# Performance work log

Measured on AMD Instinct MI355X. Metric: run time of the kernel, lower is better.

The kernel has to match this reference:

```python
import jax, jax.numpy as jnp
import numpy as np

RES = 64

TRI_TABLE = jnp.array([
    [-1,-1,-1,-1,-1,-1],[1,0,2,-1,-1,-1],[4,0,3,-1,-1,-1],[1,4,2,1,3,4],
    [3,1,5,-1,-1,-1],[2,3,0,2,5,3],[1,4,0,1,5,4],[4,2,5,-1,-1,-1],
    [4,5,2,-1,-1,-1],[4,1,0,4,5,1],[3,2,0,3,5,2],[1,3,5,-1,-1,-1],
    [4,1,2,4,3,1],[3,0,4,-1,-1,-1],[2,0,1,-1,-1,-1],[-1,-1,-1,-1,-1,-1]], dtype=jnp.int32)
NUM_TRI = jnp.array([0,1,1,2,1,2,2,1,1,2,2,1,2,1,1,0], dtype=jnp.int32)
BASE_EDGES = jnp.array([0,1,0,2,0,3,1,2,1,3,2,3], dtype=jnp.int32)


def _make_tet_grid(res):
    # Kuhn 6-tet decomposition of each cube of a (res+1)^3 grid.
    n = res + 1
    ii, jj, kk = np.meshgrid(np.arange(n), np.arange(n), np.arange(n), indexing='ij')
    verts = (np.stack([ii, jj, kk], -1).reshape(-1, 3).astype(np.float32)) / res
    def vid(i, j, k):
        return (i * n + j) * n + k
    i, j, k = np.meshgrid(np.arange(res), np.arange(res), np.arange(res), indexing='ij')
    i, j, k = i.ravel(), j.ravel(), k.ravel()
    c = [vid(i + (b & 1), j + ((b >> 1) & 1), k + ((b >> 2) & 1)) for b in range(8)]
    kuhn = [(0,1,3,7),(0,3,2,7),(0,2,6,7),(0,6,4,7),(0,4,5,7),(0,5,1,7)]
    tets = np.stack([np.stack([c[a], c[b], c[d], c[e]], -1) for (a, b, d, e) in kuhn], 1)
    return verts, tets.reshape(-1, 4).astype(np.int64)


def setup_inputs() -> dict:
    key = jax.random.key(0)
    verts, tets = _make_tet_grid(RES)
    level = jax.random.normal(key, (verts.shape[0], 1), dtype=jnp.float32)
    return {"level": level, "pos": jnp.asarray(verts), "tet": jnp.asarray(tets), "threshold": 0}


def reference(level, pos, tet, threshold):
    sdf = level - threshold                    # [N,1]
    occ = sdf[:, 0] > 0                        # [N]
    occ_fx4 = occ[tet]                         # [F,4]
    occ_sum = occ_fx4.sum(-1)
    valid = (occ_sum > 0) & (occ_sum < 4)
    vt = tet[valid]                            # [Fv,4]
    occ_valid = occ_fx4[valid]                 # [Fv,4]

    edges = jnp.sort(vt[:, BASE_EDGES].reshape(-1, 2), axis=1)   # [Fv*6,2]
    unique_edges, idx_map = jnp.unique(edges, axis=0, return_inverse=True)
    idx_map = idx_map.reshape(-1)
    mask_edges = occ[unique_edges].sum(-1) == 1                  # crossing edges
    mapping = jnp.where(mask_edges, jnp.cumsum(mask_edges) - 1, -1)
    idx_map = mapping[idx_map].reshape(-1, 6)                    # [Fv,6]
    interp_v = unique_edges[mask_edges]                          # [M,2]

    p = pos[interp_v]                                            # [M,2,3]
    s = sdf[interp_v][..., 0] * jnp.array([1.0, -1.0], dtype=sdf.dtype)  # [M,2]
    w = s[:, ::-1] / s.sum(1, keepdims=True)                     # flip / denom
    verts_out = (p * w[..., None]).sum(1)                        # [M,3]

    v_id = 2 ** jnp.arange(4, dtype=jnp.int32)
    tetindex = (occ_valid.astype(jnp.int32) * v_id).sum(-1)      # [Fv]
    num_tri = NUM_TRI[tetindex]
    m1, m2 = num_tri == 1, num_tri == 2
    f1 = jnp.take_along_axis(idx_map[m1], TRI_TABLE[tetindex[m1]][:, :3], axis=1).reshape(-1, 3)
    f2 = jnp.take_along_axis(idx_map[m2], TRI_TABLE[tetindex[m2]][:, :6], axis=1).reshape(-1, 3)
    faces = jnp.concatenate([f1, f2], axis=0)
    return verts_out, faces
```

## Files before the change

### kernel.cpp

```cpp
#include <hip/hip_runtime.h>


#define RESX 64
#define NV   65
#define NV2  4225
#define NVERT 274625
#define NCUBE 262144
#define BLOCK 256
#define NGRP 1073
#define CGRP 1024
#define NBLK1 269
#define CBLK 1024
#define FOLD (NGRP - CBLK)
#define WINW 20
#define STAGE 9216
#define M21 0x1fffffu

__constant__ int c_tri[16][6] = {
    {-1,-1,-1,-1,-1,-1},{1,0,2,-1,-1,-1},{4,0,3,-1,-1,-1},{1,4,2,1,3,4},
    {3,1,5,-1,-1,-1},{2,3,0,2,5,3},{1,4,0,1,5,4},{4,2,5,-1,-1,-1},
    {4,5,2,-1,-1,-1},{4,1,0,4,5,1},{3,2,0,3,5,2},{1,3,5,-1,-1,-1},
    {4,1,2,4,3,1},{3,0,4,-1,-1,-1},{2,0,1,-1,-1,-1},{-1,-1,-1,-1,-1,-1}};
__constant__ int c_ntri[16] = {0,1,1,2,1,2,2,1,1,2,2,1,2,1,1,0};
__constant__ int c_kuhn[6][4] = {{0,1,3,7},{0,3,2,7},{0,2,6,7},{0,6,4,7},{0,4,5,7},{0,5,1,7}};
__constant__ int c_off8[8] = {0,4225,65,4290,1,4226,66,4291};
__constant__ int c_loc[6][6] = {
    {0,0,0,1,1,3},{0,0,0,2,3,2},{0,0,0,2,2,6},
    {0,0,0,4,6,4},{0,0,0,4,4,5},{0,0,0,1,5,1}};
__constant__ int c_dir[6][6] = {
    {3,5,6,1,2,0},{5,1,6,3,0,4},{1,2,6,0,4,3},
    {2,0,6,1,3,5},{0,4,6,3,5,1},{4,3,6,0,1,2}};

typedef unsigned long long u64;
#define NTRI_PACK 0x16696994u

__device__ __forceinline__ u64 block_reduce_u64(u64 v, u64* lds) {
    int tid = threadIdx.x, lane = tid & 63, w = tid >> 6;
#pragma unroll
    for (int off = 32; off > 0; off >>= 1)
        v += __shfl_xor(v, off, 64);
    if (lane == 0) lds[w] = v;
    __syncthreads();
    if (tid == 0) lds[4] = lds[0] + lds[1] + lds[2] + lds[3];
    __syncthreads();
    return lds[4];
}

__device__ __forceinline__ unsigned block_scan_excl(unsigned val, unsigned* lds,
                                                    unsigned& block_total) {
    int tid = threadIdx.x, lane = tid & 63, w = tid >> 6;
    unsigned x = val;
#pragma unroll
    for (int off = 1; off < 64; off <<= 1) {
        unsigned y = (unsigned)__shfl_up((int)x, off, 64);
        if (lane >= off) x += y;
    }
    if (lane == 63) lds[w] = x;
    __syncthreads();
    if (tid == 0) {
        unsigned s = 0;
#pragma unroll
        for (int i = 0; i < 4; i++) { unsigned t = lds[i]; lds[i + 4] = s; s += t; }
        lds[8] = s;
    }
    __syncthreads();
    block_total = lds[8];
    return x - val + lds[4 + w];
}

__global__ void __launch_bounds__(256)
pass1(const float* __restrict__ level, const float* __restrict__ thrp,
      unsigned char* __restrict__ flagsArr, unsigned short* __restrict__ locEx,
      u64* __restrict__ bsAll) {
    int tid = threadIdx.x, lane = tid & 63, w = tid >> 6;
    int group = blockIdx.x * 4 + w;
    if (group >= NGRP) return;
    float thr = thrp[0];

    int v = group * 256 + lane * 4;
    unsigned fl[4] = {0, 0, 0, 0};
    if (v <= NVERT - 4295) {
        float r0[5], rY[5], rX[5], rXY[5];
#pragma unroll
        for (int e = 0; e < 5; e++) {
            r0[e]  = level[v + e]        - thr;
            rY[e]  = level[v + 65 + e]   - thr;
            rX[e]  = level[v + 4225 + e] - thr;
            rXY[e] = level[v + 4290 + e] - thr;
        }
        int i0 = v / NV2; int r = v - i0 * NV2; int j0 = r / NV; int k0 = r - j0 * NV;
#pragma unroll
        for (int d = 0; d < 4; d++) {
            int kk = k0 + d, jj = j0;
            if (kk > 64) { kk -= 65; jj += 1; }
            if (jj > 64) { jj -= 65; }
            bool oky = jj < RESX, okz = kk < RESX;
            bool s0 = r0[d] > 0.f;
            unsigned f = s0 ? 0x80u : 0u;
            if (okz &&        ((r0[d+1]  > 0.f) != s0)) f |= 1u;
            if (oky &&        ((rY[d]    > 0.f) != s0)) f |= 2u;
            if (oky && okz && ((rY[d+1]  > 0.f) != s0)) f |= 4u;
            if (              ((rX[d]    > 0.f) != s0)) f |= 8u;
            if (okz &&        ((rX[d+1]  > 0.f) != s0)) f |= 16u;
            if (oky &&        ((rXY[d]   > 0.f) != s0)) f |= 32u;
            if (oky && okz && ((rXY[d+1] > 0.f) != s0)) f |= 64u;
            fl[d] = f;
        }
    } else {
        const int b2d[8] = {0, 3, 1, 5, 0, 4, 2, 6};
#pragma unroll
        for (int d = 0; d < 4; d++) {
            int g = v + d;
            if (g >= NVERT) continue;
            int i = g / NV2; int r = g - i * NV2; int j = r / NV; int k = r - j * NV;
            bool okx = i < RESX, oky = j < RESX, okz = k < RESX;
            float s = level[g] - thr;
            bool s0 = s > 0.f;
            unsigned f = s0 ? 0x80u : 0u;
#pragma unroll
            for (int b = 1; b < 8; b++) {
                bool ok = (!(b & 1) || okx) && (!(b & 2) || oky) && (!(b & 4) || okz);
                if (ok) {
                    float vb = level[g + c_off8[b]] - thr;
                    if ((vb > 0.f) != s0) f |= (1u << b2d[b]);
                }
            }
            fl[d] = f;
        }
    }
    unsigned cnt[4];
#pragma unroll
    for (int d = 0; d < 4; d++) cnt[d] = __popc(fl[d] & 0x7fu);
    unsigned cth = cnt[0] + cnt[1] + cnt[2] + cnt[3];
    unsigned x = cth;
#pragma unroll
    for (int off = 1; off < 64; off <<= 1) {
        unsigned y = (unsigned)__shfl_up((int)x, off, 64);
        if (lane >= off) x += y;
    }
    unsigned wex = x - cth;
    unsigned totE = (unsigned)__shfl((int)x, 63, 64);
    if (v + 3 < NVERT) {
        *(uchar4*)(flagsArr + v) = make_uchar4((unsigned char)fl[0], (unsigned char)fl[1],
                                               (unsigned char)fl[2], (unsigned char)fl[3]);
        ushort4 e4;
        e4.x = (unsigned short)wex;
        e4.y = (unsigned short)(wex + cnt[0]);
        e4.z = (unsigned short)(wex + cnt[0] + cnt[1]);
        e4.w = (unsigned short)(wex + cnt[0] + cnt[1] + cnt[2]);
        *(ushort4*)(locEx + v) = e4;
    } else {
        unsigned e = wex;
        for (int d = 0; d < 4; d++) {
            int g = v + d;
            if (g < NVERT) {
                flagsArr[g] = (unsigned char)fl[d];
                locEx[g] = (unsigned short)e;
                e += cnt[d];
            }
        }
    }

    unsigned c1 = 0, c2 = 0;
    if (group < CGRP) {
        int c0 = group * 256 + lane * 4;
        int ci = c0 >> 12, cj = (c0 >> 6) & 63, ck = c0 & 63;
        int base = (ci * NV + cj) * NV + ck;
        float q0[5], qY[5], qX[5], qXY[5];
#pragma unroll
        for (int e = 0; e < 5; e++) {
            q0[e]  = level[base + e]        - thr;
            qY[e]  = level[base + 65 + e]   - thr;
            qX[e]  = level[base + 4225 + e] - thr;
            qXY[e] = level[base + 4290 + e] - thr;
        }
#pragma unroll
        for (int d = 0; d < 4; d++) {
            unsigned occ8 = (q0[d]   > 0.f ?   1u : 0u) | (qX[d]   > 0.f ?   2u : 0u)
                          | (qY[d]   > 0.f ?   4u : 0u) | (qXY[d]  > 0.f ?   8u : 0u)
                          | (q0[d+1] > 0.f ?  16u : 0u) | (qX[d+1] > 0.f ?  32u : 0u)
                          | (qY[d+1] > 0.f ?  64u : 0u) | (qXY[d+1]> 0.f ? 128u : 0u);
#pragma unroll
            for (int t = 0; t < 6; t++) {
                int cfg = ((occ8 >> c_kuhn[t][0]) & 1) | (((occ8 >> c_kuhn[t][1]) & 1) << 1)
                        | (((occ8 >> c_kuhn[t][2]) & 1) << 2) | (((occ8 >> c_kuhn[t][3]) & 1) << 3);
                unsigned nt = (NTRI_PACK >> (cfg << 1)) & 3u;
                c1 += (nt == 1);
                c2 += (nt == 2);
            }
        }
        unsigned pk = c1 | (c2 << 16);
#pragma unroll
        for (int off = 32; off; off >>= 1) pk += (unsigned)__shfl_xor((int)pk, off, 64);
        c1 = pk & 0xffffu; c2 = pk >> 16;
    }
    if (lane == 0)
        bsAll[group] = (u64)totE | ((u64)c1 << 16) | ((u64)c2 << 32);
}

__device__ __forceinline__ void emit_verts_group(
        int g, unsigned pE, const float* __restrict__ level, float thr,
        const unsigned char* __restrict__ flagsArr,
        const unsigned short* __restrict__ locEx,
        const u64* __restrict__ bsAll, float* stage, float* __restrict__ out,
        const float* cv ) {
    int tid = threadIdx.x;
    int gid = g * BLOCK + tid;
    float lv[8];
    if (cv == nullptr) {
        int gsafe = (gid < NVERT) ? gid : 0;
#pragma unroll
        for (int b = 0; b < 8; b++) {
            int a = gsafe + c_off8[b];
            lv[b] = level[a < NVERT ? a : 0] - thr;
        }
    } else {
#pragma unroll
        for (int b = 0; b < 8; b++) lv[b] = cv[b];
    }
    if (gid < NVERT) {
        unsigned fl = flagsArr[gid];
        if (fl & 0x7fu) {
            int i = gid / NV2; int r = gid - i * NV2; int j = r / NV; int k = r - j * NV;
            float v0 = lv[0];
            unsigned slot = locEx[gid];
            const float inv = 1.f / 64.f;
            const int d2b[7] = {4, 2, 6, 1, 5, 3, 7};
            float fi = (float)i, fj = (float)j, fk = (float)k;
#pragma unroll
            for (int d = 0; d < 7; d++) {
                if (fl & (1u << d)) {
                    const int b = d2b[d];
                    float s1 = lv[b];
                    float w1 = v0 * __builtin_amdgcn_rcpf(v0 - s1);
                    float* o = &stage[3u * slot];
                    o[0] = (fi + (float)(b & 1) * w1) * inv;
                    o[1] = (fj + (float)((b >> 1) & 1) * w1) * inv;
                    o[2] = (fk + (float)((b >> 2) & 1) * w1) * inv;
                    slot++;
                }
            }
        }
    }
    __syncthreads();
    unsigned totE = (unsigned)bsAll[g] & 0xffffu;
    float* dst = out + 3u * pE;
    unsigned n = totE * 3u;
    for (unsigned idx = tid; idx < n; idx += BLOCK)
        __builtin_nontemporal_store(stage[idx], &dst[idx]);
}

__global__ void __launch_bounds__(256)
pass2(const float* __restrict__ level, const float* __restrict__ thrp,
      const unsigned char* __restrict__ flagsArr,
      const unsigned short* __restrict__ locEx,
      const u64* __restrict__ bsAll, float* __restrict__ out) {
    __shared__ unsigned lds[9];
    __shared__ u64 lds64[5];
    __shared__ unsigned win[WINW];
    __shared__ unsigned pEw[WINW];
    __shared__ float stage[STAGE];
    int tid = threadIdx.x;
    int bid = blockIdx.x;
    int gid = bid * BLOCK + tid;
    float thr = thrp[0];
    bool hasB = (bid < FOLD);
    int gB = bid + CBLK;

    int g0 = bid << 8;
    int wci = g0 >> 12, wcj = (g0 >> 6) & 63;
    int wb = ((wci * NV + wcj) * NV) >> 8;

    unsigned lE = 0, lEp = 0, lEpB = 0, lWb = 0, l1 = 0, l1p = 0, l2p = 0;
    for (int t = tid; t < NGRP; t += BLOCK) {
        u64 a = bsAll[t];
        unsigned e  = (unsigned)a & 0xffffu;
        unsigned x1 = (unsigned)(a >> 16) & 0xffffu;
        unsigned x2 = (unsigned)(a >> 32) & 0xffffu;
        lE += e; l1 += x1;
        if (t < bid) { lEp += e; l1p += x1; l2p += x2; }
        if (t < gB)  { lEpB += e; }
        if (t < wb)  { lWb += e; }
    }
    if (tid < WINW) {
        int t = wb + tid;
        win[tid] = (t < NGRP) ? ((unsigned)bsAll[t] & 0xffffu) : 0u;
    }
    float cv[8];
    {
        int gsafe = (gid < NVERT) ? gid : 0;
#pragma unroll
        for (int b = 0; b < 8; b++) {
            int a = gsafe + c_off8[b];
            cv[b] = level[a < NVERT ? a : 0] - thr;
        }
    }
    u64 r0 = block_reduce_u64((u64)lE | ((u64)lEp << 21) | ((u64)lWb << 42), lds64);
    u64 r1 = block_reduce_u64((u64)l1 | ((u64)l1p << 21) | ((u64)l2p << 42), lds64);
    u64 r2 = block_reduce_u64((u64)lEpB, lds64);
    unsigned M    = (unsigned)r0 & M21;
    unsigned pE   = (unsigned)(r0 >> 21) & M21;
    unsigned wAcc = (unsigned)(r0 >> 42);
    unsigned C1   = (unsigned)r1 & M21;
    unsigned p1b  = (unsigned)(r1 >> 21) & M21;
    unsigned p2b  = (unsigned)(r1 >> 42);
    unsigned pEB  = (unsigned)r2;
    if (tid < WINW) {
        unsigned s = wAcc;
        for (int d = 0; d < tid; d++) s += win[d];
        pEw[tid] = s;
    }

    emit_verts_group(bid, pE, level, thr, flagsArr, locEx, bsAll, stage, out, cv);
    if (hasB) {
        __syncthreads();
        emit_verts_group(gB, pEB, level, thr, flagsArr, locEx, bsAll, stage, out,
                         nullptr);
    }
    __syncthreads();

    int ci = gid >> 12, cj = (gid >> 6) & 63, ck = gid & 63;
    int base = (ci * NV + cj) * NV + ck;
    u64 f8 = 0ull;
#pragma unroll
    for (int b = 0; b < 8; b++)
        f8 |= (u64)flagsArr[base + c_off8[b]] << (8 * b);
    unsigned occ8 = 0;
#pragma unroll
    for (int b = 0; b < 8; b++) occ8 |= (unsigned)((f8 >> (8 * b + 7)) & 1ull) << b;
    int cfgs[6], nts[6];
    unsigned c1 = 0, c2 = 0;
#pragma unroll
    for (int t = 0; t < 6; t++) {
        int cfg = ((occ8 >> c_kuhn[t][0]) & 1) | (((occ8 >> c_kuhn[t][1]) & 1) << 1)
                | (((occ8 >> c_kuhn[t][2]) & 1) << 2) | (((occ8 >> c_kuhn[t][3]) & 1) << 3);
        cfgs[t] = cfg;
        int nt = c_ntri[cfg];
        nts[t] = nt;
        c1 += (nt == 1); c2 += (nt == 2);
    }
    unsigned tot2;
    unsigned ex2 = block_scan_excl(c1 | (c2 << 16), lds, tot2);
    unsigned f1 = tot2 & 0xffffu;
    unsigned f2 = tot2 >> 16;
    unsigned l1c = ex2 & 0xffffu;
    unsigned l2c = ex2 >> 16;
    unsigned n1 = f1 * 3u;
#pragma unroll
    for (int t = 0; t < 6; t++) {
        int nt = nts[t];
        if (nt == 0) continue;
        int cfg = cfgs[t];
        unsigned basef = (nt == 1) ? (3u * l1c) : (n1 + 6u * l2c);
        int cntm = 3 * nt;
        for (int m = 0; m < cntm; m++) {
            int e = c_tri[cfg][m];
            int lc = c_loc[t][e];
            int dir = c_dir[t][e];
            int lo = base + c_off8[lc];
            unsigned flb = (unsigned)((f8 >> (8 * lc)) & 0xffull);
            unsigned rnk = pEw[(lo >> 8) - wb] + locEx[lo]
                         + __popc(flb & ((1u << dir) - 1u));
            stage[basef + (unsigned)m] = (float)rnk;
        }
        l1c += (nt == 1);
        l2c += (nt == 2);
    }
    __syncthreads();
    float* of = out + 3ull * M;
    float* o1 = of + 3u * p1b;
    for (unsigned idx = tid; idx < n1; idx += BLOCK)
        __builtin_nontemporal_store(stage[idx], &o1[idx]);
    unsigned n2 = f2 * 6u;
    float* o2 = of + 3u * (C1 + 2u * p2b);
    for (unsigned idx = tid; idx < n2; idx += BLOCK)
        __builtin_nontemporal_store(stage[n1 + idx], &o2[idx]);
}

extern "C" void kernel_launch(void* const* d_in, const int* in_sizes, int n_in,
                              void* d_out, int out_size, void* d_ws, size_t ws_size,
                              hipStream_t stream) {
    const float* level = (const float*)d_in[0];
    const float* thrp = (const float*)d_in[3];
    float* out = (float*)d_out;

    char* p = (char*)d_ws;
    unsigned char* flagsArr = (unsigned char*)p;
    p += (NVERT + 255) & ~255;
    unsigned short* locEx = (unsigned short*)p;
    p += ((sizeof(unsigned short) * NVERT) + 255) & ~255;
    u64* bsAll = (u64*)p;

    pass1<<<NBLK1, BLOCK, 0, stream>>>(level, thrp, flagsArr, locEx, bsAll);
    pass2<<<CBLK, BLOCK, 0, stream>>>(level, thrp, flagsArr, locEx, bsAll, out);
}
```

Baseline: 114.3 us.

## Fuse both passes into one persistent kernel with a software grid barrier

Replaces the two-kernel pipeline with a single kernel of 1024 blocks that computes per-vertex flags, per-block counts and triangle counts, then synchronizes through an atomic-counter grid barrier before emitting vertices and faces. Per-thread level samples and scan results are kept in registers across the barrier instead of being reloaded. The two-triangle case now computes four edge ranks and reuses them, relying on the fixed shape of the triangle table. This removes one kernel launch and the reloads between passes. In exchange it adds a memset launch and a spin barrier that depends on all 1024 blocks being co-resident; launch bounds request four blocks per SM to make that hold.

```diff
diff --git a/kernel.cpp b/kernel.cpp
--- a/kernel.cpp
+++ b/kernel.cpp
@@ -9,19 +9,18 @@
 #define BLOCK 256
 #define NGRP 1073
 #define CGRP 1024
-#define NBLK1 269
 #define CBLK 1024
 #define FOLD (NGRP - CBLK)
 #define WINW 20
 #define STAGE 9216
 #define M21 0x1fffffu
+#define NTRI_PACK 0x16696994u
 
 __constant__ int c_tri[16][6] = {
     {-1,-1,-1,-1,-1,-1},{1,0,2,-1,-1,-1},{4,0,3,-1,-1,-1},{1,4,2,1,3,4},
     {3,1,5,-1,-1,-1},{2,3,0,2,5,3},{1,4,0,1,5,4},{4,2,5,-1,-1,-1},
     {4,5,2,-1,-1,-1},{4,1,0,4,5,1},{3,2,0,3,5,2},{1,3,5,-1,-1,-1},
     {4,1,2,4,3,1},{3,0,4,-1,-1,-1},{2,0,1,-1,-1,-1},{-1,-1,-1,-1,-1,-1}};
-__constant__ int c_ntri[16] = {0,1,1,2,1,2,2,1,1,2,2,1,2,1,1,0};
 __constant__ int c_kuhn[6][4] = {{0,1,3,7},{0,3,2,7},{0,2,6,7},{0,6,4,7},{0,4,5,7},{0,5,1,7}};
 __constant__ int c_off8[8] = {0,4225,65,4290,1,4226,66,4291};
 __constant__ int c_loc[6][6] = {
@@ -32,7 +31,6 @@
     {2,0,6,1,3,5},{0,4,6,3,5,1},{4,3,6,0,1,2}};
 
 typedef unsigned long long u64;
-#define NTRI_PACK 0x16696994u
 
 __device__ __forceinline__ u64 block_reduce_u64(u64 v, u64* lds) {
     int tid = threadIdx.x, lane = tid & 63, w = tid >> 6;
@@ -68,162 +66,63 @@
     return x - val + lds[4 + w];
 }
 
-__global__ void __launch_bounds__(256)
-pass1(const float* __restrict__ level, const float* __restrict__ thrp,
-      unsigned char* __restrict__ flagsArr, unsigned short* __restrict__ locEx,
-      u64* __restrict__ bsAll) {
-    int tid = threadIdx.x, lane = tid & 63, w = tid >> 6;
-    int group = blockIdx.x * 4 + w;
-    if (group >= NGRP) return;
-    float thr = thrp[0];
-
-    int v = group * 256 + lane * 4;
-    unsigned fl[4] = {0, 0, 0, 0};
-    if (v <= NVERT - 4295) {
-        float r0[5], rY[5], rX[5], rXY[5];
-#pragma unroll
-        for (int e = 0; e < 5; e++) {
-            r0[e]  = level[v + e]        - thr;
-            rY[e]  = level[v + 65 + e]   - thr;
-            rX[e]  = level[v + 4225 + e] - thr;
-            rXY[e] = level[v + 4290 + e] - thr;
-        }
-        int i0 = v / NV2; int r = v - i0 * NV2; int j0 = r / NV; int k0 = r - j0 * NV;
-#pragma unroll
-        for (int d = 0; d < 4; d++) {
-            int kk = k0 + d, jj = j0;
-            if (kk > 64) { kk -= 65; jj += 1; }
-            if (jj > 64) { jj -= 65; }
-            bool oky = jj < RESX, okz = kk < RESX;
-            bool s0 = r0[d] > 0.f;
-            unsigned f = s0 ? 0x80u : 0u;
-            if (okz &&        ((r0[d+1]  > 0.f) != s0)) f |= 1u;
-            if (oky &&        ((rY[d]    > 0.f) != s0)) f |= 2u;
-            if (oky && okz && ((rY[d+1]  > 0.f) != s0)) f |= 4u;
-            if (              ((rX[d]    > 0.f) != s0)) f |= 8u;
-            if (okz &&        ((rX[d+1]  > 0.f) != s0)) f |= 16u;
-            if (oky &&        ((rXY[d]   > 0.f) != s0)) f |= 32u;
-            if (oky && okz && ((rXY[d+1] > 0.f) != s0)) f |= 64u;
-            fl[d] = f;
-        }
-    } else {
-        const int b2d[8] = {0, 3, 1, 5, 0, 4, 2, 6};
-#pragma unroll
-        for (int d = 0; d < 4; d++) {
-            int g = v + d;
-            if (g >= NVERT) continue;
-            int i = g / NV2; int r = g - i * NV2; int j = r / NV; int k = r - j * NV;
-            bool okx = i < RESX, oky = j < RESX, okz = k < RESX;
-            float s = level[g] - thr;
-            bool s0 = s > 0.f;
-            unsigned f = s0 ? 0x80u : 0u;
-#pragma unroll
-            for (int b = 1; b < 8; b++) {
-                bool ok = (!(b & 1) || okx) && (!(b & 2) || oky) && (!(b & 4) || okz);
-                if (ok) {
-                    float vb = level[g + c_off8[b]] - thr;
-                    if ((vb > 0.f) != s0) f |= (1u << b2d[b]);
-                }
-            }
-            fl[d] = f;
-        }
-    }
-    unsigned cnt[4];
-#pragma unroll
-    for (int d = 0; d < 4; d++) cnt[d] = __popc(fl[d] & 0x7fu);
-    unsigned cth = cnt[0] + cnt[1] + cnt[2] + cnt[3];
-    unsigned x = cth;
-#pragma unroll
-    for (int off = 1; off < 64; off <<= 1) {
-        unsigned y = (unsigned)__shfl_up((int)x, off, 64);
-        if (lane >= off) x += y;
-    }
-    unsigned wex = x - cth;
-    unsigned totE = (unsigned)__shfl((int)x, 63, 64);
-    if (v + 3 < NVERT) {
-        *(uchar4*)(flagsArr + v) = make_uchar4((unsigned char)fl[0], (unsigned char)fl[1],
-                                               (unsigned char)fl[2], (unsigned char)fl[3]);
-        ushort4 e4;
-        e4.x = (unsigned short)wex;
-        e4.y = (unsigned short)(wex + cnt[0]);
-        e4.z = (unsigned short)(wex + cnt[0] + cnt[1]);
-        e4.w = (unsigned short)(wex + cnt[0] + cnt[1] + cnt[2]);
-        *(ushort4*)(locEx + v) = e4;
-    } else {
-        unsigned e = wex;
-        for (int d = 0; d < 4; d++) {
-            int g = v + d;
-            if (g < NVERT) {
-                flagsArr[g] = (unsigned char)fl[d];
-                locEx[g] = (unsigned short)e;
-                e += cnt[d];
-            }
-        }
-    }
-
-    unsigned c1 = 0, c2 = 0;
-    if (group < CGRP) {
-        int c0 = group * 256 + lane * 4;
-        int ci = c0 >> 12, cj = (c0 >> 6) & 63, ck = c0 & 63;
-        int base = (ci * NV + cj) * NV + ck;
-        float q0[5], qY[5], qX[5], qXY[5];
-#pragma unroll
-        for (int e = 0; e < 5; e++) {
-            q0[e]  = level[base + e]        - thr;
-            qY[e]  = level[base + 65 + e]   - thr;
-            qX[e]  = level[base + 4225 + e] - thr;
-            qXY[e] = level[base + 4290 + e] - thr;
-        }
-#pragma unroll
-        for (int d = 0; d < 4; d++) {
-            unsigned occ8 = (q0[d]   > 0.f ?   1u : 0u) | (qX[d]   > 0.f ?   2u : 0u)
-                          | (qY[d]   > 0.f ?   4u : 0u) | (qXY[d]  > 0.f ?   8u : 0u)
-                          | (q0[d+1] > 0.f ?  16u : 0u) | (qX[d+1] > 0.f ?  32u : 0u)
-                          | (qY[d+1] > 0.f ?  64u : 0u) | (qXY[d+1]> 0.f ? 128u : 0u);
-#pragma unroll
-            for (int t = 0; t < 6; t++) {
-                int cfg = ((occ8 >> c_kuhn[t][0]) & 1) | (((occ8 >> c_kuhn[t][1]) & 1) << 1)
-                        | (((occ8 >> c_kuhn[t][2]) & 1) << 2) | (((occ8 >> c_kuhn[t][3]) & 1) << 3);
-                unsigned nt = (NTRI_PACK >> (cfg << 1)) & 3u;
-                c1 += (nt == 1);
-                c2 += (nt == 2);
-            }
-        }
-        unsigned pk = c1 | (c2 << 16);
-#pragma unroll
-        for (int off = 32; off; off >>= 1) pk += (unsigned)__shfl_xor((int)pk, off, 64);
-        c1 = pk & 0xffffu; c2 = pk >> 16;
-    }
-    if (lane == 0)
-        bsAll[group] = (u64)totE | ((u64)c1 << 16) | ((u64)c2 << 32);
-}
-
-__device__ __forceinline__ void emit_verts_group(
+template <bool GUARD>
+__device__ __forceinline__ unsigned vflags(const float* __restrict__ level, float thr,
+                                           int gid, float lv[8]) {
+    int gsafe = GUARD ? ((gid < NVERT) ? gid : 0) : gid;
+#pragma unroll
+    for (int b = 0; b < 8; b++) {
+        int a = gsafe + c_off8[b];
+        if (GUARD) a = (a < NVERT) ? a : 0;
+        lv[b] = level[a] - thr;
+    }
+    int i = gsafe / NV2; int r = gsafe - i * NV2; int j = r / NV; int k = r - j * NV;
+    bool okx = i < RESX, oky = j < RESX, okz = k < RESX;
+    bool s0 = lv[0] > 0.f;
+    unsigned f = s0 ? 0x80u : 0u;
+    if (okz               && ((lv[4] > 0.f) != s0)) f |= 1u;
+    if (oky               && ((lv[2] > 0.f) != s0)) f |= 2u;
+    if (oky && okz        && ((lv[6] > 0.f) != s0)) f |= 4u;
+    if (okx               && ((lv[1] > 0.f) != s0)) f |= 8u;
+    if (okx && okz        && ((lv[5] > 0.f) != s0)) f |= 16u;
+    if (okx && oky        && ((lv[3] > 0.f) != s0)) f |= 32u;
+    if (okx && oky && okz && ((lv[7] > 0.f) != s0)) f |= 64u;
+    if (GUARD && gid >= NVERT) f = 0u;
+    return f;
+}
+
+__device__ __forceinline__ void grid_sync(unsigned* cnt) {
+    __syncthreads();
+    if (threadIdx.x == 0) {
+        __threadfence();
+        __hip_atomic_fetch_add(cnt, 1u, __ATOMIC_ACQ_REL, __HIP_MEMORY_SCOPE_AGENT);
+        while (__hip_atomic_load(cnt, __ATOMIC_ACQUIRE, __HIP_MEMORY_SCOPE_AGENT) < CBLK)
+            __builtin_amdgcn_s_sleep(2);
+        __threadfence();
+    }
+    __syncthreads();
+}
+
+__device__ __forceinline__ void emit_verts_group_g(
         int g, unsigned pE, const float* __restrict__ level, float thr,
         const unsigned char* __restrict__ flagsArr,
         const unsigned short* __restrict__ locEx,
-        const u64* __restrict__ bsAll, float* stage, float* __restrict__ out,
-        const float* cv ) {
+        const u64* __restrict__ bsAll, float* stage, float* __restrict__ out) {
     int tid = threadIdx.x;
-    int gid = g * BLOCK + tid;
+    int gidv = g * BLOCK + tid;
     float lv[8];
-    if (cv == nullptr) {
-        int gsafe = (gid < NVERT) ? gid : 0;
-#pragma unroll
-        for (int b = 0; b < 8; b++) {
-            int a = gsafe + c_off8[b];
-            lv[b] = level[a < NVERT ? a : 0] - thr;
-        }
-    } else {
-#pragma unroll
-        for (int b = 0; b < 8; b++) lv[b] = cv[b];
-    }
-    if (gid < NVERT) {
-        unsigned fl = flagsArr[gid];
+    int gsafe = (gidv < NVERT) ? gidv : 0;
+#pragma unroll
+    for (int b = 0; b < 8; b++) {
+        int a = gsafe + c_off8[b];
+        lv[b] = level[a < NVERT ? a : 0] - thr;
+    }
+    if (gidv < NVERT) {
+        unsigned fl = flagsArr[gidv];
         if (fl & 0x7fu) {
-            int i = gid / NV2; int r = gid - i * NV2; int j = r / NV; int k = r - j * NV;
+            int i = gidv / NV2; int r = gidv - i * NV2; int j = r / NV; int k = r - j * NV;
             float v0 = lv[0];
-            unsigned slot = locEx[gid];
+            unsigned slot = locEx[gidv];
             const float inv = 1.f / 64.f;
             const int d2b[7] = {4, 2, 6, 1, 5, 3, 7};
             float fi = (float)i, fj = (float)j, fk = (float)k;
@@ -250,22 +149,67 @@
         __builtin_nontemporal_store(stage[idx], &dst[idx]);
 }
 
-__global__ void __launch_bounds__(256)
-pass2(const float* __restrict__ level, const float* __restrict__ thrp,
-      const unsigned char* __restrict__ flagsArr,
-      const unsigned short* __restrict__ locEx,
-      const u64* __restrict__ bsAll, float* __restrict__ out) {
+__global__ void __launch_bounds__(256, 4)
+fused(const float* __restrict__ level, const float* __restrict__ thrp,
+      unsigned char* __restrict__ flagsArr, unsigned short* __restrict__ locEx,
+      u64* __restrict__ bsAll, float* __restrict__ out,
+      unsigned* __restrict__ barCnt) {
     __shared__ unsigned lds[9];
     __shared__ u64 lds64[5];
     __shared__ unsigned win[WINW];
     __shared__ unsigned pEw[WINW];
     __shared__ float stage[STAGE];
-    int tid = threadIdx.x;
-    int bid = blockIdx.x;
+    int tid = threadIdx.x, bid = blockIdx.x;
     int gid = bid * BLOCK + tid;
     float thr = thrp[0];
     bool hasB = (bid < FOLD);
     int gB = bid + CBLK;
+
+    float lv[8];
+    unsigned fl = vflags<false>(level, thr, gid, lv);
+    unsigned cntv = __popc(fl & 0x7fu);
+    unsigned totE;
+    unsigned slot = block_scan_excl(cntv, lds, totE);
+    flagsArr[gid] = (unsigned char)fl;
+    locEx[gid] = (unsigned short)slot;
+
+    if (hasB) {
+        float lvB[8];
+        int gid2 = gB * BLOCK + tid;
+        unsigned fB = vflags<true>(level, thr, gid2, lvB);
+        unsigned cB = __popc(fB & 0x7fu);
+        unsigned totB;
+        unsigned sB = block_scan_excl(cB, lds, totB);
+        if (gid2 < NVERT) {
+            flagsArr[gid2] = (unsigned char)fB;
+            locEx[gid2] = (unsigned short)sB;
+        }
+        if (tid == 0) bsAll[gB] = (u64)totB;
+    }
+
+    int ci = gid >> 12, cj = (gid >> 6) & 63, ck = gid & 63;
+    int cbase = (ci * NV + cj) * NV + ck;
+    unsigned occ8 = 0;
+#pragma unroll
+    for (int b = 0; b < 8; b++)
+        occ8 |= (((level[cbase + c_off8[b]] - thr) > 0.f) ? 1u : 0u) << b;
+    unsigned ex2, tot2u;
+    {
+        unsigned c1 = 0, c2 = 0;
+#pragma unroll
+        for (int t = 0; t < 6; t++) {
+            int cfg = ((occ8 >> c_kuhn[t][0]) & 1) | (((occ8 >> c_kuhn[t][1]) & 1) << 1)
+                    | (((occ8 >> c_kuhn[t][2]) & 1) << 2) | (((occ8 >> c_kuhn[t][3]) & 1) << 3);
+            unsigned nt = (NTRI_PACK >> (cfg << 1)) & 3u;
+            c1 += (nt == 1); c2 += (nt == 2);
+        }
+        ex2 = block_scan_excl(c1 | (c2 << 16), lds, tot2u);
+    }
+    if (tid == 0)
+        bsAll[bid] = (u64)totE | ((u64)(tot2u & 0xffffu) << 16)
+                   | ((u64)(tot2u >> 16) << 32);
+
+    grid_sync(barCnt);
 
     int g0 = bid << 8;
     int wci = g0 >> 12, wcj = (g0 >> 6) & 63;
@@ -285,15 +229,6 @@
     if (tid < WINW) {
         int t = wb + tid;
         win[tid] = (t < NGRP) ? ((unsigned)bsAll[t] & 0xffffu) : 0u;
-    }
-    float cv[8];
-    {
-        int gsafe = (gid < NVERT) ? gid : 0;
-#pragma unroll
-        for (int b = 0; b < 8; b++) {
-            int a = gsafe + c_off8[b];
-            cv[b] = level[a < NVERT ? a : 0] - thr;
-        }
     }
     u64 r0 = block_reduce_u64((u64)lE | ((u64)lEp << 21) | ((u64)lWb << 42), lds64);
     u64 r1 = block_reduce_u64((u64)l1 | ((u64)l1p << 21) | ((u64)l2p << 42), lds64);
@@ -311,60 +246,77 @@
         pEw[tid] = s;
     }
 
-    emit_verts_group(bid, pE, level, thr, flagsArr, locEx, bsAll, stage, out, cv);
+    if (fl & 0x7fu) {
+        int i = gid / NV2; int r = gid - i * NV2; int j = r / NV; int k = r - j * NV;
+        float v0 = lv[0];
+        unsigned s = slot;
+        const float inv = 1.f / 64.f;
+        const int d2b[7] = {4, 2, 6, 1, 5, 3, 7};
+        float fi = (float)i, fj = (float)j, fk = (float)k;
+#pragma unroll
+        for (int d = 0; d < 7; d++) {
+            if (fl & (1u << d)) {
+                const int b = d2b[d];
+                float s1 = lv[b];
+                float w1 = v0 * __builtin_amdgcn_rcpf(v0 - s1);
+                float* o = &stage[3u * s];
+                o[0] = (fi + (float)(b & 1) * w1) * inv;
+                o[1] = (fj + (float)((b >> 1) & 1) * w1) * inv;
+                o[2] = (fk + (float)((b >> 2) & 1) * w1) * inv;
+                s++;
+            }
+        }
+    }
+    __syncthreads();
+    {
+        float* dst = out + 3u * pE;
+        unsigned n = totE * 3u;
+        for (unsigned idx = tid; idx < n; idx += BLOCK)
+            __builtin_nontemporal_store(stage[idx], &dst[idx]);
+    }
     if (hasB) {
         __syncthreads();
-        emit_verts_group(gB, pEB, level, thr, flagsArr, locEx, bsAll, stage, out,
-                         nullptr);
-    }
-    __syncthreads();
-
-    int ci = gid >> 12, cj = (gid >> 6) & 63, ck = gid & 63;
-    int base = (ci * NV + cj) * NV + ck;
+        emit_verts_group_g(gB, pEB, level, thr, flagsArr, locEx, bsAll, stage, out);
+    }
+    __syncthreads();
+
     u64 f8 = 0ull;
 #pragma unroll
     for (int b = 0; b < 8; b++)
-        f8 |= (u64)flagsArr[base + c_off8[b]] << (8 * b);
-    unsigned occ8 = 0;
-#pragma unroll
-    for (int b = 0; b < 8; b++) occ8 |= (unsigned)((f8 >> (8 * b + 7)) & 1ull) << b;
-    int cfgs[6], nts[6];
-    unsigned c1 = 0, c2 = 0;
+        f8 |= (u64)flagsArr[cbase + c_off8[b]] << (8 * b);
+    unsigned f1 = tot2u & 0xffffu;
+    unsigned f2 = tot2u >> 16;
+    unsigned l1c = ex2 & 0xffffu;
+    unsigned l2c = ex2 >> 16;
+    unsigned n1 = f1 * 3u;
 #pragma unroll
     for (int t = 0; t < 6; t++) {
         int cfg = ((occ8 >> c_kuhn[t][0]) & 1) | (((occ8 >> c_kuhn[t][1]) & 1) << 1)
                 | (((occ8 >> c_kuhn[t][2]) & 1) << 2) | (((occ8 >> c_kuhn[t][3]) & 1) << 3);
-        cfgs[t] = cfg;
-        int nt = c_ntri[cfg];
-        nts[t] = nt;
-        c1 += (nt == 1); c2 += (nt == 2);
-    }
-    unsigned tot2;
-    unsigned ex2 = block_scan_excl(c1 | (c2 << 16), lds, tot2);
-    unsigned f1 = tot2 & 0xffffu;
-    unsigned f2 = tot2 >> 16;
-    unsigned l1c = ex2 & 0xffffu;
-    unsigned l2c = ex2 >> 16;
-    unsigned n1 = f1 * 3u;
-#pragma unroll
-    for (int t = 0; t < 6; t++) {
-        int nt = nts[t];
+        unsigned nt = (NTRI_PACK >> (cfg << 1)) & 3u;
         if (nt == 0) continue;
-        int cfg = cfgs[t];
-        unsigned basef = (nt == 1) ? (3u * l1c) : (n1 + 6u * l2c);
-        int cntm = 3 * nt;
-        for (int m = 0; m < cntm; m++) {
-            int e = c_tri[cfg][m];
+        auto rank = [&](int e) -> float {
             int lc = c_loc[t][e];
             int dir = c_dir[t][e];
-            int lo = base + c_off8[lc];
+            int lo = cbase + c_off8[lc];
             unsigned flb = (unsigned)((f8 >> (8 * lc)) & 0xffull);
-            unsigned rnk = pEw[(lo >> 8) - wb] + locEx[lo]
-                         + __popc(flb & ((1u << dir) - 1u));
-            stage[basef + (unsigned)m] = (float)rnk;
-        }
-        l1c += (nt == 1);
-        l2c += (nt == 2);
+            return (float)(pEw[(lo >> 8) - wb] + locEx[lo]
+                           + __popc(flb & ((1u << dir) - 1u)));
+        };
+        float ra = rank(c_tri[cfg][0]);
+        float rb = rank(c_tri[cfg][1]);
+        float rc = rank(c_tri[cfg][2]);
+        if (nt == 1) {
+            unsigned bfo = 3u * l1c;
+            stage[bfo]     = ra; stage[bfo + 1] = rb; stage[bfo + 2] = rc;
+            l1c++;
+        } else {
+            float rd = rank(c_tri[cfg][4]);
+            unsigned bfo = n1 + 6u * l2c;
+            stage[bfo]     = ra; stage[bfo + 1] = rb; stage[bfo + 2] = rc;
+            stage[bfo + 3] = ra; stage[bfo + 4] = rd; stage[bfo + 5] = rb;
+            l2c++;
+        }
     }
     __syncthreads();
     float* of = out + 3ull * M;
@@ -390,7 +342,10 @@
     unsigned short* locEx = (unsigned short*)p;
     p += ((sizeof(unsigned short) * NVERT) + 255) & ~255;
     u64* bsAll = (u64*)p;
-
-    pass1<<<NBLK1, BLOCK, 0, stream>>>(level, thrp, flagsArr, locEx, bsAll);
-    pass2<<<CBLK, BLOCK, 0, stream>>>(level, thrp, flagsArr, locEx, bsAll, out);
-}
+    p += ((sizeof(u64) * NGRP) + 255) & ~255;
+    unsigned* barCnt = (unsigned*)p;
+
+    hipMemsetAsync(barCnt, 0, sizeof(unsigned), stream);
+    fused<<<CBLK, BLOCK, 0, stream>>>(level, thrp, flagsArr, locEx, bsAll, out,
+                                      barCnt);
+}
```

Result: slower. 170.6 us (+49.2%).

## Add separate prefix-scan kernel and write outputs directly without LDS staging

Applied to the files above, without the earlier changes.

Adds a single-block scan kernel that computes per-group exclusive prefixes and totals once, so each pass2 block no longer loops over all groups and runs three block reductions. Pass2 also drops its 36KB LDS staging buffer and the syncs around it, writing vertices and faces straight to global memory with nontemporal stores. Face triangle counts now come from a packed constant. The cost is an extra kernel launch and scattered, less coalesced global stores in place of contiguous staged writes, while the smaller LDS footprint allows more blocks per CU.

```diff
diff --git a/kernel.cpp b/kernel.cpp
--- a/kernel.cpp
+++ b/kernel.cpp
@@ -13,8 +13,8 @@
 #define CBLK 1024
 #define FOLD (NGRP - CBLK)
 #define WINW 20
-#define STAGE 9216
 #define M21 0x1fffffu
+#define NTRI_PACK 0x16696994u
 
 __constant__ int c_tri[16][6] = {
     {-1,-1,-1,-1,-1,-1},{1,0,2,-1,-1,-1},{4,0,3,-1,-1,-1},{1,4,2,1,3,4},
@@ -32,19 +32,6 @@
     {2,0,6,1,3,5},{0,4,6,3,5,1},{4,3,6,0,1,2}};
 
 typedef unsigned long long u64;
-#define NTRI_PACK 0x16696994u
-
-__device__ __forceinline__ u64 block_reduce_u64(u64 v, u64* lds) {
-    int tid = threadIdx.x, lane = tid & 63, w = tid >> 6;
-#pragma unroll
-    for (int off = 32; off > 0; off >>= 1)
-        v += __shfl_xor(v, off, 64);
-    if (lane == 0) lds[w] = v;
-    __syncthreads();
-    if (tid == 0) lds[4] = lds[0] + lds[1] + lds[2] + lds[3];
-    __syncthreads();
-    return lds[4];
-}
 
 __device__ __forceinline__ unsigned block_scan_excl(unsigned val, unsigned* lds,
                                                     unsigned& block_total) {
@@ -198,32 +185,64 @@
         bsAll[group] = (u64)totE | ((u64)c1 << 16) | ((u64)c2 << 32);
 }
 
-__device__ __forceinline__ void emit_verts_group(
-        int g, unsigned pE, const float* __restrict__ level, float thr,
+__global__ void __launch_bounds__(1024)
+scanK(const u64* __restrict__ bsAll, uint4* __restrict__ pre) {
+    __shared__ u64 lws[16];
+    int tid = threadIdx.x, lane = tid & 63, w = tid >> 6;
+    int i0 = 2 * tid, i1 = 2 * tid + 1;
+    u64 a0 = (i0 < NGRP) ? bsAll[i0] : 0ull;
+    u64 a1 = (i1 < NGRP) ? bsAll[i1] : 0ull;
+    u64 v0 = (a0 & 0xffffull) | (((a0 >> 16) & 0xffffull) << 21)
+           | (((a0 >> 32) & 0xffffull) << 42);
+    u64 v1 = (a1 & 0xffffull) | (((a1 >> 16) & 0xffffull) << 21)
+           | (((a1 >> 32) & 0xffffull) << 42);
+    u64 s = v0 + v1;
+    u64 x = s;
+#pragma unroll
+    for (int off = 1; off < 64; off <<= 1) {
+        u64 y = __shfl_up(x, off, 64);
+        if (lane >= off) x += y;
+    }
+    if (lane == 63) lws[w] = x;
+    __syncthreads();
+    if (tid == 0) {
+        u64 acc = 0;
+#pragma unroll
+        for (int i = 0; i < 16; i++) { u64 t = lws[i]; lws[i] = acc; acc += t; }
+    }
+    __syncthreads();
+    u64 ex = x - s + lws[w];
+    if (i0 < NGRP)
+        pre[i0] = make_uint4((unsigned)(ex & M21), (unsigned)((ex >> 21) & M21),
+                             (unsigned)(ex >> 42), 0u);
+    u64 e1 = ex + v0;
+    if (i1 < NGRP)
+        pre[i1] = make_uint4((unsigned)(e1 & M21), (unsigned)((e1 >> 21) & M21),
+                             (unsigned)(e1 >> 42), 0u);
+    if (tid == 1023) {
+        u64 tot = ex + s;
+        pre[NGRP] = make_uint4((unsigned)(tot & M21), (unsigned)((tot >> 21) & M21),
+                               (unsigned)(tot >> 42), 0u);
+    }
+}
+
+__device__ __forceinline__ void emit_verts_group_d(
+        int gidv, unsigned pE, const float* __restrict__ level, float thr,
         const unsigned char* __restrict__ flagsArr,
-        const unsigned short* __restrict__ locEx,
-        const u64* __restrict__ bsAll, float* stage, float* __restrict__ out,
-        const float* cv ) {
-    int tid = threadIdx.x;
-    int gid = g * BLOCK + tid;
+        const unsigned short* __restrict__ locEx, float* __restrict__ out) {
     float lv[8];
-    if (cv == nullptr) {
-        int gsafe = (gid < NVERT) ? gid : 0;
-#pragma unroll
-        for (int b = 0; b < 8; b++) {
-            int a = gsafe + c_off8[b];
-            lv[b] = level[a < NVERT ? a : 0] - thr;
-        }
-    } else {
-#pragma unroll
-        for (int b = 0; b < 8; b++) lv[b] = cv[b];
-    }
-    if (gid < NVERT) {
-        unsigned fl = flagsArr[gid];
+    int gsafe = (gidv < NVERT) ? gidv : 0;
+#pragma unroll
+    for (int b = 0; b < 8; b++) {
+        int a = gsafe + c_off8[b];
+        lv[b] = level[a < NVERT ? a : 0] - thr;
+    }
+    if (gidv < NVERT) {
+        unsigned fl = flagsArr[gidv];
         if (fl & 0x7fu) {
-            int i = gid / NV2; int r = gid - i * NV2; int j = r / NV; int k = r - j * NV;
+            int i = gidv / NV2; int r = gidv - i * NV2; int j = r / NV; int k = r - j * NV;
             float v0 = lv[0];
-            unsigned slot = locEx[gid];
+            unsigned slot = pE + locEx[gidv];
             const float inv = 1.f / 64.f;
             const int d2b[7] = {4, 2, 6, 1, 5, 3, 7};
             float fi = (float)i, fj = (float)j, fk = (float)k;
@@ -233,33 +252,24 @@
                     const int b = d2b[d];
                     float s1 = lv[b];
                     float w1 = v0 * __builtin_amdgcn_rcpf(v0 - s1);
-                    float* o = &stage[3u * slot];
-                    o[0] = (fi + (float)(b & 1) * w1) * inv;
-                    o[1] = (fj + (float)((b >> 1) & 1) * w1) * inv;
-                    o[2] = (fk + (float)((b >> 2) & 1) * w1) * inv;
+                    float* o = out + 3u * slot;
+                    __builtin_nontemporal_store((fi + (float)(b & 1) * w1) * inv, o);
+                    __builtin_nontemporal_store((fj + (float)((b >> 1) & 1) * w1) * inv, o + 1);
+                    __builtin_nontemporal_store((fk + (float)((b >> 2) & 1) * w1) * inv, o + 2);
                     slot++;
                 }
             }
         }
     }
-    __syncthreads();
-    unsigned totE = (unsigned)bsAll[g] & 0xffffu;
-    float* dst = out + 3u * pE;
-    unsigned n = totE * 3u;
-    for (unsigned idx = tid; idx < n; idx += BLOCK)
-        __builtin_nontemporal_store(stage[idx], &dst[idx]);
 }
 
 __global__ void __launch_bounds__(256)
 pass2(const float* __restrict__ level, const float* __restrict__ thrp,
       const unsigned char* __restrict__ flagsArr,
       const unsigned short* __restrict__ locEx,
-      const u64* __restrict__ bsAll, float* __restrict__ out) {
+      const uint4* __restrict__ pre, float* __restrict__ out) {
     __shared__ unsigned lds[9];
-    __shared__ u64 lds64[5];
-    __shared__ unsigned win[WINW];
     __shared__ unsigned pEw[WINW];
-    __shared__ float stage[STAGE];
     int tid = threadIdx.x;
     int bid = blockIdx.x;
     int gid = bid * BLOCK + tid;
@@ -267,57 +277,23 @@
     bool hasB = (bid < FOLD);
     int gB = bid + CBLK;
 
+    uint4 pb = pre[bid];
+    uint4 pt = pre[NGRP];
+    unsigned pE  = pb.x, p1b = pb.y, p2b = pb.z;
+    unsigned M   = pt.x, C1  = pt.y;
+
     int g0 = bid << 8;
     int wci = g0 >> 12, wcj = (g0 >> 6) & 63;
     int wb = ((wci * NV + wcj) * NV) >> 8;
-
-    unsigned lE = 0, lEp = 0, lEpB = 0, lWb = 0, l1 = 0, l1p = 0, l2p = 0;
-    for (int t = tid; t < NGRP; t += BLOCK) {
-        u64 a = bsAll[t];
-        unsigned e  = (unsigned)a & 0xffffu;
-        unsigned x1 = (unsigned)(a >> 16) & 0xffffu;
-        unsigned x2 = (unsigned)(a >> 32) & 0xffffu;
-        lE += e; l1 += x1;
-        if (t < bid) { lEp += e; l1p += x1; l2p += x2; }
-        if (t < gB)  { lEpB += e; }
-        if (t < wb)  { lWb += e; }
-    }
     if (tid < WINW) {
         int t = wb + tid;
-        win[tid] = (t < NGRP) ? ((unsigned)bsAll[t] & 0xffffu) : 0u;
-    }
-    float cv[8];
-    {
-        int gsafe = (gid < NVERT) ? gid : 0;
-#pragma unroll
-        for (int b = 0; b < 8; b++) {
-            int a = gsafe + c_off8[b];
-            cv[b] = level[a < NVERT ? a : 0] - thr;
-        }
-    }
-    u64 r0 = block_reduce_u64((u64)lE | ((u64)lEp << 21) | ((u64)lWb << 42), lds64);
-    u64 r1 = block_reduce_u64((u64)l1 | ((u64)l1p << 21) | ((u64)l2p << 42), lds64);
-    u64 r2 = block_reduce_u64((u64)lEpB, lds64);
-    unsigned M    = (unsigned)r0 & M21;
-    unsigned pE   = (unsigned)(r0 >> 21) & M21;
-    unsigned wAcc = (unsigned)(r0 >> 42);
-    unsigned C1   = (unsigned)r1 & M21;
-    unsigned p1b  = (unsigned)(r1 >> 21) & M21;
-    unsigned p2b  = (unsigned)(r1 >> 42);
-    unsigned pEB  = (unsigned)r2;
-    if (tid < WINW) {
-        unsigned s = wAcc;
-        for (int d = 0; d < tid; d++) s += win[d];
-        pEw[tid] = s;
-    }
-
-    emit_verts_group(bid, pE, level, thr, flagsArr, locEx, bsAll, stage, out, cv);
-    if (hasB) {
-        __syncthreads();
-        emit_verts_group(gB, pEB, level, thr, flagsArr, locEx, bsAll, stage, out,
-                         nullptr);
-    }
-    __syncthreads();
+        pEw[tid] = (t <= NGRP) ? pre[t].x : M;
+    }
+
+    emit_verts_group_d(gid, pE, level, thr, flagsArr, locEx, out);
+    if (hasB)
+        emit_verts_group_d(gB * BLOCK + tid, pre[gB].x, level, thr, flagsArr,
+                           locEx, out);
 
     int ci = gid >> 12, cj = (gid >> 6) & 63, ck = gid & 63;
     int base = (ci * NV + cj) * NV + ck;
@@ -328,53 +304,57 @@
     unsigned occ8 = 0;
 #pragma unroll
     for (int b = 0; b < 8; b++) occ8 |= (unsigned)((f8 >> (8 * b + 7)) & 1ull) << b;
-    int cfgs[6], nts[6];
+    int cfgs[6];
     unsigned c1 = 0, c2 = 0;
 #pragma unroll
     for (int t = 0; t < 6; t++) {
         int cfg = ((occ8 >> c_kuhn[t][0]) & 1) | (((occ8 >> c_kuhn[t][1]) & 1) << 1)
                 | (((occ8 >> c_kuhn[t][2]) & 1) << 2) | (((occ8 >> c_kuhn[t][3]) & 1) << 3);
         cfgs[t] = cfg;
-        int nt = c_ntri[cfg];
-        nts[t] = nt;
+        unsigned nt = (NTRI_PACK >> (cfg << 1)) & 3u;
         c1 += (nt == 1); c2 += (nt == 2);
     }
     unsigned tot2;
     unsigned ex2 = block_scan_excl(c1 | (c2 << 16), lds, tot2);
-    unsigned f1 = tot2 & 0xffffu;
-    unsigned f2 = tot2 >> 16;
     unsigned l1c = ex2 & 0xffffu;
     unsigned l2c = ex2 >> 16;
-    unsigned n1 = f1 * 3u;
+    float* of = out + 3ull * M;
+    float* o1 = of + 3u * p1b;
+    float* o2 = of + 3u * (C1 + 2u * p2b);
 #pragma unroll
     for (int t = 0; t < 6; t++) {
-        int nt = nts[t];
+        int cfg = cfgs[t];
+        unsigned nt = (NTRI_PACK >> (cfg << 1)) & 3u;
         if (nt == 0) continue;
-        int cfg = cfgs[t];
-        unsigned basef = (nt == 1) ? (3u * l1c) : (n1 + 6u * l2c);
-        int cntm = 3 * nt;
-        for (int m = 0; m < cntm; m++) {
-            int e = c_tri[cfg][m];
+        auto rank = [&](int e) -> float {
             int lc = c_loc[t][e];
             int dir = c_dir[t][e];
             int lo = base + c_off8[lc];
             unsigned flb = (unsigned)((f8 >> (8 * lc)) & 0xffull);
-            unsigned rnk = pEw[(lo >> 8) - wb] + locEx[lo]
-                         + __popc(flb & ((1u << dir) - 1u));
-            stage[basef + (unsigned)m] = (float)rnk;
-        }
-        l1c += (nt == 1);
-        l2c += (nt == 2);
-    }
-    __syncthreads();
-    float* of = out + 3ull * M;
-    float* o1 = of + 3u * p1b;
-    for (unsigned idx = tid; idx < n1; idx += BLOCK)
-        __builtin_nontemporal_store(stage[idx], &o1[idx]);
-    unsigned n2 = f2 * 6u;
-    float* o2 = of + 3u * (C1 + 2u * p2b);
-    for (unsigned idx = tid; idx < n2; idx += BLOCK)
-        __builtin_nontemporal_store(stage[n1 + idx], &o2[idx]);
+            return (float)(pEw[(lo >> 8) - wb] + locEx[lo]
+                           + __popc(flb & ((1u << dir) - 1u)));
+        };
+        float ra = rank(c_tri[cfg][0]);
+        float rb = rank(c_tri[cfg][1]);
+        float rc = rank(c_tri[cfg][2]);
+        if (nt == 1) {
+            float* p = o1 + 3u * l1c;
+            __builtin_nontemporal_store(ra, p);
+            __builtin_nontemporal_store(rb, p + 1);
+            __builtin_nontemporal_store(rc, p + 2);
+            l1c++;
+        } else {
+            float rd = rank(c_tri[cfg][4]);
+            float* p = o2 + 6u * l2c;
+            __builtin_nontemporal_store(ra, p);
+            __builtin_nontemporal_store(rb, p + 1);
+            __builtin_nontemporal_store(rc, p + 2);
+            __builtin_nontemporal_store(ra, p + 3);
+            __builtin_nontemporal_store(rd, p + 4);
+            __builtin_nontemporal_store(rb, p + 5);
+            l2c++;
+        }
+    }
 }
 
 extern "C" void kernel_launch(void* const* d_in, const int* in_sizes, int n_in,
@@ -390,7 +370,10 @@
     unsigned short* locEx = (unsigned short*)p;
     p += ((sizeof(unsigned short) * NVERT) + 255) & ~255;
     u64* bsAll = (u64*)p;
+    p += ((sizeof(u64) * NGRP) + 255) & ~255;
+    uint4* pre = (uint4*)p;
 
     pass1<<<NBLK1, BLOCK, 0, stream>>>(level, thrp, flagsArr, locEx, bsAll);
-    pass2<<<CBLK, BLOCK, 0, stream>>>(level, thrp, flagsArr, locEx, bsAll, out);
-}
+    scanK<<<1, 1024, 0, stream>>>(bsAll, pre);
+    pass2<<<CBLK, BLOCK, 0, stream>>>(level, thrp, flagsArr, locEx, pre, out);
+}
```

New measurement: 155.1 us. 1.36x slower.
